# Performance work log

Measured on AMD Instinct MI355X. Metric: run time of the kernel, lower is better.

Reference implementation:

```python
import jax, jax.numpy as jnp
import numpy as np

N = 50000   # nodes
E = 800000  # edges
H = 64      # hidden channels
EPS = 1e-16  # PyG softmax denominator epsilon


def _ptconv(x, pos, src, dst, W_src, W_dst, W_val, W_pos, b_pos):
    """PyG PointTransformerConv: per-edge gather, positional MLP, vector
    attention (segment softmax over edges grouped by dst), scatter-sum.
    edge_index convention: src = j (neighbor), dst = i (center)."""
    a_src = x @ W_src          # [N,H] alpha_j projection
    a_dst = x @ W_dst          # [N,H] alpha_i projection
    v = x @ W_val              # [N,H] values
    # relative positional encoding: pos_nn(pos_i - pos_j), [E,H]
    delta = (pos[dst] - pos[src]) @ W_pos + b_pos
    alpha = a_dst[dst] - a_src[src] + delta           # [E,H]
    # numerically-stable vector softmax over variable-size neighborhoods
    m = jax.lax.stop_gradient(jax.ops.segment_max(alpha, dst, num_segments=N))
    e = jnp.exp(alpha - m[dst])
    s = jax.ops.segment_sum(e, dst, num_segments=N)
    attn = e / (s[dst] + EPS)                         # [E,H]
    return jax.ops.segment_sum(attn * (v[src] + delta), dst, num_segments=N)


def setup_inputs() -> dict:
    key = jax.random.key(0)
    ks = jax.random.split(key, 16)
    x = jax.random.normal(ks[0], (N, 3), dtype=jnp.float32)
    pos = jax.random.normal(ks[1], (N, 3), dtype=jnp.float32)
    edge_index = jax.random.randint(ks[2], (2, E), 0, N)
    batch = jnp.zeros((N,), dtype=jnp.int32)

    def lin(k, i, o):
        return (jax.random.normal(k, (i, o), dtype=jnp.float32)
                * np.float32(1.0 / np.sqrt(i)))

    return {
        "x": x, "pos": pos, "edge_index": edge_index, "batch": batch,
        # conv1 (in=3 -> H)
        "W1_src": lin(ks[3], 3, H), "W1_dst": lin(ks[4], 3, H),
        "W1_val": lin(ks[5], 3, H),
        "W1_pos": lin(ks[6], 3, H), "b1_pos": jnp.zeros((H,), jnp.float32),
        # conv2 (H -> H)
        "W2_src": lin(ks[7], H, H), "W2_dst": lin(ks[8], H, H),
        "W2_val": lin(ks[9], H, H),
        "W2_pos": lin(ks[10], 3, H), "b2_pos": jnp.zeros((H,), jnp.float32),
        # MLP head
        "W_fc1": lin(ks[11], H, H // 2), "b_fc1": jnp.zeros((H // 2,), jnp.float32),
        "W_fc2": lin(ks[12], H // 2, 1), "b_fc2": jnp.zeros((1,), jnp.float32),
    }


def reference(x, pos, edge_index, batch,
              W1_src, W1_dst, W1_val, W1_pos, b1_pos,
              W2_src, W2_dst, W2_val, W2_pos, b2_pos,
              W_fc1, b_fc1, W_fc2, b_fc2):
    src, dst = edge_index[0], edge_index[1]
    h = jax.nn.relu(_ptconv(x, pos, src, dst, W1_src, W1_dst, W1_val, W1_pos, b1_pos))
    h = jax.nn.relu(_ptconv(h, pos, src, dst, W2_src, W2_dst, W2_val, W2_pos, b2_pos))
    h = jax.nn.relu(h @ W_fc1 + b_fc1)
    return h @ W_fc2 + b_fc2  # [N, 1]
```

## Files before the change

### kernel.cpp

```cpp
#include <hip/hip_runtime.h>
#include <hip/hip_fp16.h>
#include <math.h>


#define HDIM 64

__global__ void zero_int_kernel(int* __restrict__ p, int n) {
    int i = blockIdx.x * blockDim.x + threadIdx.x;
    if (i < n) p[i] = 0;
}

__global__ void hist_rank_kernel(const int* __restrict__ dst, int* __restrict__ count,
                                 int* __restrict__ rank, int E) {
    int e = blockIdx.x * blockDim.x + threadIdx.x;
    if (e < E) rank[e] = atomicAdd(&count[dst[e]], 1);
}

__global__ void __launch_bounds__(256) scan_sum_kernel(
        const int* __restrict__ count, int* __restrict__ blocksum, int n) {
    __shared__ int wsum[4];
    int t = blockIdx.x * 256 + threadIdx.x;
    int base = t * 4;
    int s = 0;
    if (base + 3 < n) {
        int4 c = *(const int4*)&count[base];
        s = c.x + c.y + c.z + c.w;
    } else {
        for (int i = base; i < n; ++i) s += count[i];
    }
    #pragma unroll
    for (int off = 32; off >= 1; off >>= 1) s += __shfl_down(s, off);
    int lane = threadIdx.x & 63, wid = threadIdx.x >> 6;
    if (lane == 0) wsum[wid] = s;
    __syncthreads();
    if (threadIdx.x == 0)
        blocksum[blockIdx.x] = wsum[0] + wsum[1] + wsum[2] + wsum[3];
}

__global__ void scan_base_kernel(int* __restrict__ blocksum, int* __restrict__ offsets,
                                 int nblocks, int n) {
    int lane = threadIdx.x;
    int v = (lane < nblocks) ? blocksum[lane] : 0;
    int inc = v;
    #pragma unroll
    for (int off = 1; off < 64; off <<= 1) {
        int t = __shfl_up(inc, off);
        if (lane >= off) inc += t;
    }
    if (lane < nblocks) blocksum[lane] = inc - v;
    if (lane == 63) offsets[n] = inc;
}

__global__ void __launch_bounds__(256) scan_emit_kernel(
        const int* __restrict__ count, const int* __restrict__ blockbase,
        int* __restrict__ offsets, int n) {
    __shared__ int wpre[4];
    int t = blockIdx.x * 256 + threadIdx.x;
    int base = t * 4;
    int4 c = make_int4(0, 0, 0, 0);
    if (base + 3 < n) {
        c = *(const int4*)&count[base];
    } else {
        if (base + 0 < n) c.x = count[base + 0];
        if (base + 1 < n) c.y = count[base + 1];
        if (base + 2 < n) c.z = count[base + 2];
    }
    int tsum = c.x + c.y + c.z + c.w;
    int inc = tsum;
    int lane = threadIdx.x & 63, wid = threadIdx.x >> 6;
    #pragma unroll
    for (int off = 1; off < 64; off <<= 1) {
        int t2 = __shfl_up(inc, off);
        if (lane >= off) inc += t2;
    }
    if (lane == 63) wpre[wid] = inc;
    __syncthreads();
    int wbase = 0;
    for (int wq = 0; wq < wid; ++wq) wbase += wpre[wq];
    int excl = blockbase[blockIdx.x] + wbase + (inc - tsum);
    if (base + 0 < n) offsets[base + 0] = excl;
    if (base + 1 < n) offsets[base + 1] = excl + c.x;
    if (base + 2 < n) offsets[base + 2] = excl + c.x + c.y;
    if (base + 3 < n) offsets[base + 3] = excl + c.x + c.y + c.z;
}

__global__ void scatter_kernel(const int* __restrict__ src, const int* __restrict__ dst,
                               const int* __restrict__ rank, const int* __restrict__ offsets,
                               int* __restrict__ sorted_src, int E) {
    int e = blockIdx.x * blockDim.x + threadIdx.x;
    if (e < E) sorted_src[offsets[dst[e]] + rank[e]] = src[e];
}

__global__ void proj1_kernel(const float* __restrict__ x, const float* __restrict__ pos,
                             const float* __restrict__ Wsrc, const float* __restrict__ Wval,
                             const float* __restrict__ Wpos,
                             __half2* __restrict__ g, int N) {
    int t = blockIdx.x * blockDim.x + threadIdx.x;
    int node = t >> 6, c = t & 63;
    if (node >= N) return;
    float x0 = x[node * 3 + 0], x1 = x[node * 3 + 1], x2 = x[node * 3 + 2];
    float p0 = pos[node * 3 + 0], p1 = pos[node * 3 + 1], p2 = pos[node * 3 + 2];
    float as = fmaf(x0, Wsrc[c], fmaf(x1, Wsrc[64 + c], x2 * Wsrc[128 + c]));
    float vv = fmaf(x0, Wval[c], fmaf(x1, Wval[64 + c], x2 * Wval[128 + c]));
    float cc = fmaf(p0, Wpos[c], fmaf(p1, Wpos[64 + c], p2 * Wpos[128 + c]));
    g[node * 64 + c] = __float22half2_rn(make_float2(as + cc, vv - cc));
}

__global__ void __launch_bounds__(256) proj2_kernel(
        const float* __restrict__ h, const float* __restrict__ pos,
        const float* __restrict__ Wsrc, const float* __restrict__ Wval,
        const float* __restrict__ Wpos,
        __half2* __restrict__ g, int N) {
    __shared__ float Wsh[2 * 64 * 64];
    __shared__ float hrow[4][64];
    int tid = threadIdx.x;
    for (int idx = tid; idx < 4096; idx += 256) {
        Wsh[idx] = Wsrc[idx];
        Wsh[4096 + idx] = Wval[idx];
    }
    __syncthreads();
    int lane = tid & 63, wid = tid >> 6;
    float wp0 = Wpos[lane], wp1 = Wpos[64 + lane], wp2 = Wpos[128 + lane];
    int stride = gridDim.x * 4;
    for (int node = blockIdx.x * 4 + wid; node < N; node += stride) {
        hrow[wid][lane] = h[node * 64 + lane];
        float as = 0.f, vv = 0.f;
        #pragma unroll 8
        for (int k = 0; k < 64; ++k) {
            float hk = hrow[wid][k];
            as = fmaf(hk, Wsh[k * 64 + lane], as);
            vv = fmaf(hk, Wsh[4096 + k * 64 + lane], vv);
        }
        float p0 = pos[node * 3 + 0], p1 = pos[node * 3 + 1], p2 = pos[node * 3 + 2];
        float cc = fmaf(p0, wp0, fmaf(p1, wp1, p2 * wp2));
        g[node * 64 + lane] = __float22half2_rn(make_float2(as + cc, vv - cc));
    }
}

__device__ __forceinline__ void edge_acc(float d, __half2 gh, float& s, float& num) {
    float2 gv = __half22float2(gh);
    float ev = __expf(d - gv.x);
    s += ev;
    num = fmaf(ev, gv.y + d, num);
}

template <bool HEAD>
__global__ void __launch_bounds__(256) conv_edge_kernel(
        const float* __restrict__ pos,
        const int* __restrict__ offsets,
        const int* __restrict__ sorted_src,
        const __half2* __restrict__ g,
        const float* __restrict__ Wpos, const float* __restrict__ bpos,
        const float* __restrict__ Wfc1, const float* __restrict__ bfc1,
        const float* __restrict__ Wfc2, const float* __restrict__ bfc2,
        float* __restrict__ outbuf, int N) {
    int lane = threadIdx.x & 63;
    int wid = threadIdx.x >> 6;
    int node = __builtin_amdgcn_readfirstlane(blockIdx.x * 4 + wid);
    if (node >= N) return;

    float pdx = pos[node * 3 + 0], pdy = pos[node * 3 + 1], pdz = pos[node * 3 + 2];
    float d = fmaf(pdx, Wpos[lane],
              fmaf(pdy, Wpos[64 + lane],
              fmaf(pdz, Wpos[128 + lane], bpos[lane])));
    int beg = offsets[node], end = offsets[node + 1];

    float s0 = 0.f, n0 = 0.f, s1 = 0.f, n1 = 0.f;
    int e = beg;
    int aligned = min((beg + 3) & ~3, end);
    for (; e < aligned; ++e) {
        int i0 = __builtin_amdgcn_readfirstlane(sorted_src[e]);
        edge_acc(d, g[(size_t)i0 * 64 + lane], s0, n0);
    }
    for (; e + 4 <= end; e += 4) {
        int4 ii = *(const int4*)&sorted_src[e];
        int i0 = __builtin_amdgcn_readfirstlane(ii.x);
        int i1 = __builtin_amdgcn_readfirstlane(ii.y);
        int i2 = __builtin_amdgcn_readfirstlane(ii.z);
        int i3 = __builtin_amdgcn_readfirstlane(ii.w);
        __half2 g0 = g[(size_t)i0 * 64 + lane];
        __half2 g1 = g[(size_t)i1 * 64 + lane];
        __half2 g2 = g[(size_t)i2 * 64 + lane];
        __half2 g3 = g[(size_t)i3 * 64 + lane];
        edge_acc(d, g0, s0, n0);
        edge_acc(d, g1, s1, n1);
        edge_acc(d, g2, s0, n0);
        edge_acc(d, g3, s1, n1);
    }
    for (; e < end; ++e) {
        int i0 = __builtin_amdgcn_readfirstlane(sorted_src[e]);
        edge_acc(d, g[(size_t)i0 * 64 + lane], s0, n0);
    }
    float s = s0 + s1;
    float num = n0 + n1;
    float hval = fmaxf(num / (s + 1e-16f), 0.f);

    if (!HEAD) {
        outbuf[node * 64 + lane] = hval;
    } else {
        __shared__ float hsh[4][64];
        hsh[wid][lane] = hval;
        float t = 0.f;
        if (lane < 32) {
            #pragma unroll
            for (int k = 0; k < 64; ++k) t = fmaf(hsh[wid][k], Wfc1[k * 32 + lane], t);
            t += bfc1[lane];
            t = fmaxf(t, 0.f);
            t *= Wfc2[lane];
        }
        #pragma unroll
        for (int off = 32; off >= 1; off >>= 1) t += __shfl_down(t, off);
        if (lane == 0) outbuf[node] = t + bfc2[0];
    }
}

extern "C" void kernel_launch(void* const* d_in, const int* in_sizes, int n_in,
                              void* d_out, int out_size, void* d_ws, size_t ws_size,
                              hipStream_t stream) {
    const float* x   = (const float*)d_in[0];
    const float* pos = (const float*)d_in[1];
    const int* eidx  = (const int*)d_in[2];
    const float* W1_src = (const float*)d_in[4];
    const float* W1_val = (const float*)d_in[6];
    const float* W1_pos = (const float*)d_in[7];
    const float* b1_pos = (const float*)d_in[8];
    const float* W2_src = (const float*)d_in[9];
    const float* W2_val = (const float*)d_in[11];
    const float* W2_pos = (const float*)d_in[12];
    const float* b2_pos = (const float*)d_in[13];
    const float* W_fc1  = (const float*)d_in[14];
    const float* b_fc1  = (const float*)d_in[15];
    const float* W_fc2  = (const float*)d_in[16];
    const float* b_fc2  = (const float*)d_in[17];

    const int N = in_sizes[0] / 3;
    const int E = in_sizes[2] / 2;
    const int* src = eidx;
    const int* dst = eidx + E;

    char* w = (char*)d_ws;
    auto carve = [&](size_t bytes) -> void* {
        void* p = (void*)w;
        w += (bytes + 255) & ~size_t(255);
        return p;
    };
    const int nsb = (N + 1023) / 1024;
    int*     count      = (int*)carve((size_t)N * 4);
    int*     offsets    = (int*)carve((size_t)(N + 1) * 4);
    int*     blocksum   = (int*)carve((size_t)nsb * 4);
    int*     rank       = (int*)carve((size_t)E * 4);
    int*     sorted_src = (int*)carve((size_t)E * 4);
    __half2* g          = (__half2*)carve((size_t)N * HDIM * 4);
    float*   h          = (float*)carve((size_t)N * HDIM * 4);

    zero_int_kernel<<<(N + 255) / 256, 256, 0, stream>>>(count, N);
    hist_rank_kernel<<<(E + 255) / 256, 256, 0, stream>>>(dst, count, rank, E);
    scan_sum_kernel<<<nsb, 256, 0, stream>>>(count, blocksum, N);
    scan_base_kernel<<<1, 64, 0, stream>>>(blocksum, offsets, nsb, N);
    scan_emit_kernel<<<nsb, 256, 0, stream>>>(count, blocksum, offsets, N);
    scatter_kernel<<<(E + 255) / 256, 256, 0, stream>>>(src, dst, rank, offsets,
                                                        sorted_src, E);

    proj1_kernel<<<(N * 64 + 255) / 256, 256, 0, stream>>>(x, pos, W1_src, W1_val,
                                                           W1_pos, g, N);
    conv_edge_kernel<false><<<(N + 3) / 4, 256, 0, stream>>>(
        pos, offsets, sorted_src, g, W1_pos, b1_pos,
        W_fc1, b_fc1, W_fc2, b_fc2, h, N);

    proj2_kernel<<<1024, 256, 0, stream>>>(h, pos, W2_src, W2_val, W2_pos, g, N);
    conv_edge_kernel<true><<<(N + 3) / 4, 256, 0, stream>>>(
        pos, offsets, sorted_src, g, W2_pos, b2_pos,
        W_fc1, b_fc1, W_fc2, b_fc2, (float*)d_out, N);
}
```

Baseline: 277.5 us.

## Fuse projection stages into edge kernels and merge scan/histogram launches

Fuses the layer-2 projection into the layer-1 edge aggregation kernel, so h never goes to global memory; the matmul reads from shuffles and half2 weights held in shared memory. Merges the histogram with the layer-1 projection and folds the scan-base step into scan_emit, which cuts the launch count. Also pre-scales logits by log2e so the inner loop can use exp2f, unrolls the edge loop by 8, and loads the head weights into shared memory. In exchange, W2 weights are now stored in fp16, the fused kernel uses more shared memory per block, and the scan fold assumes nsb is at most 64.

```diff
diff --git a/kernel.cpp b/kernel.cpp
--- a/kernel.cpp
+++ b/kernel.cpp
@@ -3,24 +3,34 @@
 #include <math.h>
 
 
-#define HDIM 64
-
-__global__ void zero_int_kernel(int* __restrict__ p, int n) {
-    int i = blockIdx.x * blockDim.x + threadIdx.x;
-    if (i < n) p[i] = 0;
-}
-
-__global__ void hist_rank_kernel(const int* __restrict__ dst, int* __restrict__ count,
-                                 int* __restrict__ rank, int E) {
-    int e = blockIdx.x * blockDim.x + threadIdx.x;
-    if (e < E) rank[e] = atomicAdd(&count[dst[e]], 1);
+#define LOG2E 1.44269504088896340736f
+
+__global__ void __launch_bounds__(256) hist_proj1_kernel(
+        const int* __restrict__ dst, int* __restrict__ count, int* __restrict__ rank,
+        const float* __restrict__ x, const float* __restrict__ pos,
+        const float* __restrict__ W1_src, const float* __restrict__ W1_val,
+        const float* __restrict__ W1_pos,
+        __half2* __restrict__ g1, int N, int E) {
+    int gtid = blockIdx.x * 256 + threadIdx.x;
+    int gsz = gridDim.x * 256;
+    for (int e = gtid; e < E; e += gsz)
+        rank[e] = atomicAdd(&count[dst[e]], 1);
+    for (int t = gtid; t < N * 64; t += gsz) {
+        int node = t >> 6, c = t & 63;
+        float x0 = x[node * 3 + 0], x1 = x[node * 3 + 1], x2 = x[node * 3 + 2];
+        float p0 = pos[node * 3 + 0], p1 = pos[node * 3 + 1], p2 = pos[node * 3 + 2];
+        float as = fmaf(x0, W1_src[c], fmaf(x1, W1_src[64 + c], x2 * W1_src[128 + c]));
+        float vv = fmaf(x0, W1_val[c], fmaf(x1, W1_val[64 + c], x2 * W1_val[128 + c]));
+        float cc = fmaf(p0, W1_pos[c], fmaf(p1, W1_pos[64 + c], p2 * W1_pos[128 + c]));
+        g1[t] = __floats2half2_rn((as + cc) * LOG2E, vv - cc);
+    }
 }
 
 __global__ void __launch_bounds__(256) scan_sum_kernel(
         const int* __restrict__ count, int* __restrict__ blocksum, int n) {
     __shared__ int wsum[4];
-    int t = blockIdx.x * 256 + threadIdx.x;
-    int base = t * 4;
+    int tid = threadIdx.x;
+    int base = (blockIdx.x * 256 + tid) * 4;
     int s = 0;
     if (base + 3 < n) {
         int4 c = *(const int4*)&count[base];
@@ -30,33 +40,30 @@
     }
     #pragma unroll
     for (int off = 32; off >= 1; off >>= 1) s += __shfl_down(s, off);
-    int lane = threadIdx.x & 63, wid = threadIdx.x >> 6;
+    int lane = tid & 63, wid = tid >> 6;
     if (lane == 0) wsum[wid] = s;
     __syncthreads();
-    if (threadIdx.x == 0)
-        blocksum[blockIdx.x] = wsum[0] + wsum[1] + wsum[2] + wsum[3];
-}
-
-__global__ void scan_base_kernel(int* __restrict__ blocksum, int* __restrict__ offsets,
-                                 int nblocks, int n) {
-    int lane = threadIdx.x;
-    int v = (lane < nblocks) ? blocksum[lane] : 0;
-    int inc = v;
-    #pragma unroll
-    for (int off = 1; off < 64; off <<= 1) {
-        int t = __shfl_up(inc, off);
-        if (lane >= off) inc += t;
-    }
-    if (lane < nblocks) blocksum[lane] = inc - v;
-    if (lane == 63) offsets[n] = inc;
+    if (tid == 0) blocksum[blockIdx.x] = wsum[0] + wsum[1] + wsum[2] + wsum[3];
 }
 
 __global__ void __launch_bounds__(256) scan_emit_kernel(
-        const int* __restrict__ count, const int* __restrict__ blockbase,
-        int* __restrict__ offsets, int n) {
+        const int* __restrict__ count, const int* __restrict__ blocksum,
+        int* __restrict__ offsets, int n, int nsb) {
     __shared__ int wpre[4];
-    int t = blockIdx.x * 256 + threadIdx.x;
-    int base = t * 4;
+    __shared__ int sbase[2];
+    int tid = threadIdx.x, lane = tid & 63, wid = tid >> 6;
+    if (tid < 64) {
+        int v = (lane < nsb) ? blocksum[lane] : 0;
+        int inc = v;
+        #pragma unroll
+        for (int off = 1; off < 64; off <<= 1) {
+            int t2 = __shfl_up(inc, off);
+            if (lane >= off) inc += t2;
+        }
+        if (lane == (int)blockIdx.x) sbase[0] = inc - v;
+        if (lane == nsb - 1) sbase[1] = inc;
+    }
+    int base = (blockIdx.x * 256 + tid) * 4;
     int4 c = make_int4(0, 0, 0, 0);
     if (base + 3 < n) {
         c = *(const int4*)&count[base];
@@ -67,7 +74,6 @@
     }
     int tsum = c.x + c.y + c.z + c.w;
     int inc = tsum;
-    int lane = threadIdx.x & 63, wid = threadIdx.x >> 6;
     #pragma unroll
     for (int off = 1; off < 64; off <<= 1) {
         int t2 = __shfl_up(inc, off);
@@ -76,142 +82,165 @@
     if (lane == 63) wpre[wid] = inc;
     __syncthreads();
     int wbase = 0;
-    for (int wq = 0; wq < wid; ++wq) wbase += wpre[wq];
-    int excl = blockbase[blockIdx.x] + wbase + (inc - tsum);
+    for (int q = 0; q < wid; ++q) wbase += wpre[q];
+    int excl = sbase[0] + wbase + (inc - tsum);
     if (base + 0 < n) offsets[base + 0] = excl;
     if (base + 1 < n) offsets[base + 1] = excl + c.x;
     if (base + 2 < n) offsets[base + 2] = excl + c.x + c.y;
     if (base + 3 < n) offsets[base + 3] = excl + c.x + c.y + c.z;
-}
-
-__global__ void scatter_kernel(const int* __restrict__ src, const int* __restrict__ dst,
-                               const int* __restrict__ rank, const int* __restrict__ offsets,
-                               int* __restrict__ sorted_src, int E) {
-    int e = blockIdx.x * blockDim.x + threadIdx.x;
+    if (blockIdx.x == 0 && tid == 0) offsets[n] = sbase[1];
+}
+
+__global__ void __launch_bounds__(256) scatter_kernel(
+        const int* __restrict__ src, const int* __restrict__ dst,
+        const int* __restrict__ rank, const int* __restrict__ offsets,
+        int* __restrict__ sorted_src, int E) {
+    int e = blockIdx.x * 256 + threadIdx.x;
     if (e < E) sorted_src[offsets[dst[e]] + rank[e]] = src[e];
 }
 
-__global__ void proj1_kernel(const float* __restrict__ x, const float* __restrict__ pos,
-                             const float* __restrict__ Wsrc, const float* __restrict__ Wval,
-                             const float* __restrict__ Wpos,
-                             __half2* __restrict__ g, int N) {
-    int t = blockIdx.x * blockDim.x + threadIdx.x;
-    int node = t >> 6, c = t & 63;
-    if (node >= N) return;
-    float x0 = x[node * 3 + 0], x1 = x[node * 3 + 1], x2 = x[node * 3 + 2];
-    float p0 = pos[node * 3 + 0], p1 = pos[node * 3 + 1], p2 = pos[node * 3 + 2];
-    float as = fmaf(x0, Wsrc[c], fmaf(x1, Wsrc[64 + c], x2 * Wsrc[128 + c]));
-    float vv = fmaf(x0, Wval[c], fmaf(x1, Wval[64 + c], x2 * Wval[128 + c]));
-    float cc = fmaf(p0, Wpos[c], fmaf(p1, Wpos[64 + c], p2 * Wpos[128 + c]));
-    g[node * 64 + c] = __float22half2_rn(make_float2(as + cc, vv - cc));
-}
-
-__global__ void __launch_bounds__(256) proj2_kernel(
-        const float* __restrict__ h, const float* __restrict__ pos,
-        const float* __restrict__ Wsrc, const float* __restrict__ Wval,
-        const float* __restrict__ Wpos,
-        __half2* __restrict__ g, int N) {
-    __shared__ float Wsh[2 * 64 * 64];
-    __shared__ float hrow[4][64];
-    int tid = threadIdx.x;
-    for (int idx = tid; idx < 4096; idx += 256) {
-        Wsh[idx] = Wsrc[idx];
-        Wsh[4096 + idx] = Wval[idx];
-    }
-    __syncthreads();
-    int lane = tid & 63, wid = tid >> 6;
-    float wp0 = Wpos[lane], wp1 = Wpos[64 + lane], wp2 = Wpos[128 + lane];
-    int stride = gridDim.x * 4;
-    for (int node = blockIdx.x * 4 + wid; node < N; node += stride) {
-        hrow[wid][lane] = h[node * 64 + lane];
-        float as = 0.f, vv = 0.f;
-        #pragma unroll 8
-        for (int k = 0; k < 64; ++k) {
-            float hk = hrow[wid][k];
-            as = fmaf(hk, Wsh[k * 64 + lane], as);
-            vv = fmaf(hk, Wsh[4096 + k * 64 + lane], vv);
-        }
-        float p0 = pos[node * 3 + 0], p1 = pos[node * 3 + 1], p2 = pos[node * 3 + 2];
-        float cc = fmaf(p0, wp0, fmaf(p1, wp1, p2 * wp2));
-        g[node * 64 + lane] = __float22half2_rn(make_float2(as + cc, vv - cc));
-    }
-}
-
-__device__ __forceinline__ void edge_acc(float d, __half2 gh, float& s, float& num) {
-    float2 gv = __half22float2(gh);
-    float ev = __expf(d - gv.x);
+__device__ __forceinline__ void eacc(float d2, float dv, __half2 gh,
+                                     float& s, float& num) {
+    float ax = __low2float(gh);
+    float vv = __high2float(gh);
+    float ev = exp2f(d2 - ax);
     s += ev;
-    num = fmaf(ev, gv.y + d, num);
-}
-
-template <bool HEAD>
-__global__ void __launch_bounds__(256) conv_edge_kernel(
-        const float* __restrict__ pos,
-        const int* __restrict__ offsets,
-        const int* __restrict__ sorted_src,
-        const __half2* __restrict__ g,
-        const float* __restrict__ Wpos, const float* __restrict__ bpos,
-        const float* __restrict__ Wfc1, const float* __restrict__ bfc1,
-        const float* __restrict__ Wfc2, const float* __restrict__ bfc2,
-        float* __restrict__ outbuf, int N) {
-    int lane = threadIdx.x & 63;
-    int wid = threadIdx.x >> 6;
-    int node = __builtin_amdgcn_readfirstlane(blockIdx.x * 4 + wid);
-    if (node >= N) return;
-
-    float pdx = pos[node * 3 + 0], pdy = pos[node * 3 + 1], pdz = pos[node * 3 + 2];
-    float d = fmaf(pdx, Wpos[lane],
-              fmaf(pdy, Wpos[64 + lane],
-              fmaf(pdz, Wpos[128 + lane], bpos[lane])));
+    num = fmaf(ev, vv + dv, num);
+}
+
+__device__ __forceinline__ float edge_node(
+        int node, int laneoff,
+        const int* __restrict__ offsets, const int* __restrict__ ss,
+        const char* __restrict__ gbase, float d2, float dv) {
     int beg = offsets[node], end = offsets[node + 1];
-
     float s0 = 0.f, n0 = 0.f, s1 = 0.f, n1 = 0.f;
     int e = beg;
     int aligned = min((beg + 3) & ~3, end);
     for (; e < aligned; ++e) {
-        int i0 = __builtin_amdgcn_readfirstlane(sorted_src[e]);
-        edge_acc(d, g[(size_t)i0 * 64 + lane], s0, n0);
+        int i0 = __builtin_amdgcn_readfirstlane(ss[e]);
+        __half2 g0 = *(const __half2*)(gbase + (((size_t)(unsigned)i0) << 8) + laneoff);
+        eacc(d2, dv, g0, s0, n0);
+    }
+    for (; e + 8 <= end; e += 8) {
+        int4 ia = *(const int4*)(ss + e);
+        int4 ib = *(const int4*)(ss + e + 4);
+        int i0 = __builtin_amdgcn_readfirstlane(ia.x);
+        int i1 = __builtin_amdgcn_readfirstlane(ia.y);
+        int i2 = __builtin_amdgcn_readfirstlane(ia.z);
+        int i3 = __builtin_amdgcn_readfirstlane(ia.w);
+        int i4 = __builtin_amdgcn_readfirstlane(ib.x);
+        int i5 = __builtin_amdgcn_readfirstlane(ib.y);
+        int i6 = __builtin_amdgcn_readfirstlane(ib.z);
+        int i7 = __builtin_amdgcn_readfirstlane(ib.w);
+        __half2 g0 = *(const __half2*)(gbase + (((size_t)(unsigned)i0) << 8) + laneoff);
+        __half2 g1 = *(const __half2*)(gbase + (((size_t)(unsigned)i1) << 8) + laneoff);
+        __half2 g2 = *(const __half2*)(gbase + (((size_t)(unsigned)i2) << 8) + laneoff);
+        __half2 g3 = *(const __half2*)(gbase + (((size_t)(unsigned)i3) << 8) + laneoff);
+        __half2 g4 = *(const __half2*)(gbase + (((size_t)(unsigned)i4) << 8) + laneoff);
+        __half2 g5 = *(const __half2*)(gbase + (((size_t)(unsigned)i5) << 8) + laneoff);
+        __half2 g6 = *(const __half2*)(gbase + (((size_t)(unsigned)i6) << 8) + laneoff);
+        __half2 g7 = *(const __half2*)(gbase + (((size_t)(unsigned)i7) << 8) + laneoff);
+        eacc(d2, dv, g0, s0, n0);
+        eacc(d2, dv, g1, s1, n1);
+        eacc(d2, dv, g2, s0, n0);
+        eacc(d2, dv, g3, s1, n1);
+        eacc(d2, dv, g4, s0, n0);
+        eacc(d2, dv, g5, s1, n1);
+        eacc(d2, dv, g6, s0, n0);
+        eacc(d2, dv, g7, s1, n1);
     }
     for (; e + 4 <= end; e += 4) {
-        int4 ii = *(const int4*)&sorted_src[e];
-        int i0 = __builtin_amdgcn_readfirstlane(ii.x);
-        int i1 = __builtin_amdgcn_readfirstlane(ii.y);
-        int i2 = __builtin_amdgcn_readfirstlane(ii.z);
-        int i3 = __builtin_amdgcn_readfirstlane(ii.w);
-        __half2 g0 = g[(size_t)i0 * 64 + lane];
-        __half2 g1 = g[(size_t)i1 * 64 + lane];
-        __half2 g2 = g[(size_t)i2 * 64 + lane];
-        __half2 g3 = g[(size_t)i3 * 64 + lane];
-        edge_acc(d, g0, s0, n0);
-        edge_acc(d, g1, s1, n1);
-        edge_acc(d, g2, s0, n0);
-        edge_acc(d, g3, s1, n1);
+        int4 ia = *(const int4*)(ss + e);
+        int i0 = __builtin_amdgcn_readfirstlane(ia.x);
+        int i1 = __builtin_amdgcn_readfirstlane(ia.y);
+        int i2 = __builtin_amdgcn_readfirstlane(ia.z);
+        int i3 = __builtin_amdgcn_readfirstlane(ia.w);
+        __half2 g0 = *(const __half2*)(gbase + (((size_t)(unsigned)i0) << 8) + laneoff);
+        __half2 g1 = *(const __half2*)(gbase + (((size_t)(unsigned)i1) << 8) + laneoff);
+        __half2 g2 = *(const __half2*)(gbase + (((size_t)(unsigned)i2) << 8) + laneoff);
+        __half2 g3 = *(const __half2*)(gbase + (((size_t)(unsigned)i3) << 8) + laneoff);
+        eacc(d2, dv, g0, s0, n0);
+        eacc(d2, dv, g1, s1, n1);
+        eacc(d2, dv, g2, s0, n0);
+        eacc(d2, dv, g3, s1, n1);
     }
     for (; e < end; ++e) {
-        int i0 = __builtin_amdgcn_readfirstlane(sorted_src[e]);
-        edge_acc(d, g[(size_t)i0 * 64 + lane], s0, n0);
-    }
-    float s = s0 + s1;
-    float num = n0 + n1;
-    float hval = fmaxf(num / (s + 1e-16f), 0.f);
-
-    if (!HEAD) {
-        outbuf[node * 64 + lane] = hval;
-    } else {
-        __shared__ float hsh[4][64];
-        hsh[wid][lane] = hval;
-        float t = 0.f;
-        if (lane < 32) {
-            #pragma unroll
-            for (int k = 0; k < 64; ++k) t = fmaf(hsh[wid][k], Wfc1[k * 32 + lane], t);
-            t += bfc1[lane];
-            t = fmaxf(t, 0.f);
-            t *= Wfc2[lane];
-        }
-        #pragma unroll
-        for (int off = 32; off >= 1; off >>= 1) t += __shfl_down(t, off);
-        if (lane == 0) outbuf[node] = t + bfc2[0];
-    }
+        int i0 = __builtin_amdgcn_readfirstlane(ss[e]);
+        __half2 g0 = *(const __half2*)(gbase + (((size_t)(unsigned)i0) << 8) + laneoff);
+        eacc(d2, dv, g0, s0, n0);
+    }
+    return fmaxf((n0 + n1) / (s0 + s1 + 1e-16f), 0.f);
+}
+
+__global__ void __launch_bounds__(256, 8) e1p2_kernel(
+        const float* __restrict__ pos,
+        const int* __restrict__ offsets, const int* __restrict__ sorted_src,
+        const __half2* __restrict__ g1,
+        const float* __restrict__ W1_pos, const float* __restrict__ b1_pos,
+        const float* __restrict__ W2_src, const float* __restrict__ W2_val,
+        const float* __restrict__ W2_pos,
+        __half2* __restrict__ g2, int N) {
+    __shared__ __half2 Wsh[4096];
+    int tid = threadIdx.x, lane = tid & 63, wid = tid >> 6;
+    for (int idx = tid; idx < 4096; idx += 256)
+        Wsh[idx] = __floats2half2_rn(W2_src[idx], W2_val[idx]);
+    __syncthreads();
+
+    int node = blockIdx.x * 4 + wid;
+    if (node >= N) return;
+
+    float p0 = pos[node * 3 + 0], p1 = pos[node * 3 + 1], p2 = pos[node * 3 + 2];
+    float dpos = fmaf(p0, W1_pos[lane],
+                 fmaf(p1, W1_pos[64 + lane], p2 * W1_pos[128 + lane]));
+    float hval = edge_node(node, lane * 4, offsets, sorted_src,
+                           (const char*)g1, dpos * LOG2E, dpos + b1_pos[lane]);
+    float as = 0.f, vv = 0.f;
+    #pragma unroll 16
+    for (int k = 0; k < 64; ++k) {
+        float hk = __shfl(hval, k);
+        float2 wk = __half22float2(Wsh[k * 64 + lane]);
+        as = fmaf(hk, wk.x, as);
+        vv = fmaf(hk, wk.y, vv);
+    }
+    float cc = fmaf(p0, W2_pos[lane],
+               fmaf(p1, W2_pos[64 + lane], p2 * W2_pos[128 + lane]));
+    g2[node * 64 + lane] = __floats2half2_rn((as + cc) * LOG2E, vv - cc);
+}
+
+__global__ void __launch_bounds__(256, 8) e2head_kernel(
+        const float* __restrict__ pos,
+        const int* __restrict__ offsets, const int* __restrict__ sorted_src,
+        const __half2* __restrict__ g2,
+        const float* __restrict__ W2_pos, const float* __restrict__ b2_pos,
+        const float* __restrict__ Wfc1, const float* __restrict__ bfc1,
+        const float* __restrict__ Wfc2, const float* __restrict__ bfc2,
+        float* __restrict__ out, int N) {
+    __shared__ float Wfc1sh[64 * 32];
+    __shared__ float hsh[4][64];
+    int tid = threadIdx.x, lane = tid & 63, wid = tid >> 6;
+    for (int idx = tid; idx < 2048; idx += 256) Wfc1sh[idx] = Wfc1[idx];
+    __syncthreads();
+
+    int node = blockIdx.x * 4 + wid;
+    if (node >= N) return;
+
+    float p0 = pos[node * 3 + 0], p1 = pos[node * 3 + 1], p2 = pos[node * 3 + 2];
+    float dpos = fmaf(p0, W2_pos[lane],
+                 fmaf(p1, W2_pos[64 + lane], p2 * W2_pos[128 + lane]));
+    float hval = edge_node(node, lane * 4, offsets, sorted_src,
+                           (const char*)g2, dpos * LOG2E, dpos + b2_pos[lane]);
+    hsh[wid][lane] = hval;
+    int c = lane & 31, kh = (lane >> 5) * 32;
+    float t2 = 0.f;
+    #pragma unroll 8
+    for (int k = 0; k < 32; ++k)
+        t2 = fmaf(hsh[wid][kh + k], Wfc1sh[(kh + k) * 32 + c], t2);
+    t2 += __shfl_down(t2, 32);
+    t2 = fmaxf(t2 + bfc1[c], 0.f) * Wfc2[c];
+    t2 = (lane < 32) ? t2 : 0.f;
+    #pragma unroll
+    for (int off = 16; off >= 1; off >>= 1) t2 += __shfl_down(t2, off);
+    if (lane == 0) out[node] = t2 + bfc2[0];
 }
 
 extern "C" void kernel_launch(void* const* d_in, const int* in_sizes, int n_in,
@@ -237,6 +266,7 @@
     const int E = in_sizes[2] / 2;
     const int* src = eidx;
     const int* dst = eidx + E;
+    const int nsb = (N + 1023) / 1024;
 
     char* w = (char*)d_ws;
     auto carve = [&](size_t bytes) -> void* {
@@ -244,31 +274,24 @@
         w += (bytes + 255) & ~size_t(255);
         return p;
     };
-    const int nsb = (N + 1023) / 1024;
     int*     count      = (int*)carve((size_t)N * 4);
     int*     offsets    = (int*)carve((size_t)(N + 1) * 4);
-    int*     blocksum   = (int*)carve((size_t)nsb * 4);
+    int*     blocksum   = (int*)carve((size_t)64 * 4);
     int*     rank       = (int*)carve((size_t)E * 4);
     int*     sorted_src = (int*)carve((size_t)E * 4);
-    __half2* g          = (__half2*)carve((size_t)N * HDIM * 4);
-    float*   h          = (float*)carve((size_t)N * HDIM * 4);
-
-    zero_int_kernel<<<(N + 255) / 256, 256, 0, stream>>>(count, N);
-    hist_rank_kernel<<<(E + 255) / 256, 256, 0, stream>>>(dst, count, rank, E);
+    __half2* g1         = (__half2*)carve((size_t)N * 64 * 4);
+    __half2* g2         = (__half2*)carve((size_t)N * 64 * 4);
+
+    hipMemsetAsync(count, 0, (size_t)N * 4, stream);
+    hist_proj1_kernel<<<(N * 64 + 255) / 256, 256, 0, stream>>>(
+        dst, count, rank, x, pos, W1_src, W1_val, W1_pos, g1, N, E);
     scan_sum_kernel<<<nsb, 256, 0, stream>>>(count, blocksum, N);
-    scan_base_kernel<<<1, 64, 0, stream>>>(blocksum, offsets, nsb, N);
-    scan_emit_kernel<<<nsb, 256, 0, stream>>>(count, blocksum, offsets, N);
+    scan_emit_kernel<<<nsb, 256, 0, stream>>>(count, blocksum, offsets, N, nsb);
     scatter_kernel<<<(E + 255) / 256, 256, 0, stream>>>(src, dst, rank, offsets,
                                                         sorted_src, E);
-
-    proj1_kernel<<<(N * 64 + 255) / 256, 256, 0, stream>>>(x, pos, W1_src, W1_val,
-                                                           W1_pos, g, N);
-    conv_edge_kernel<false><<<(N + 3) / 4, 256, 0, stream>>>(
-        pos, offsets, sorted_src, g, W1_pos, b1_pos,
-        W_fc1, b_fc1, W_fc2, b_fc2, h, N);
-
-    proj2_kernel<<<1024, 256, 0, stream>>>(h, pos, W2_src, W2_val, W2_pos, g, N);
-    conv_edge_kernel<true><<<(N + 3) / 4, 256, 0, stream>>>(
-        pos, offsets, sorted_src, g, W2_pos, b2_pos,
+    e1p2_kernel<<<(N + 3) / 4, 256, 0, stream>>>(
+        pos, offsets, sorted_src, g1, W1_pos, b1_pos, W2_src, W2_val, W2_pos, g2, N);
+    e2head_kernel<<<(N + 3) / 4, 256, 0, stream>>>(
+        pos, offsets, sorted_src, g2, W2_pos, b2_pos,
         W_fc1, b_fc1, W_fc2, b_fc2, (float*)d_out, N);
 }
```

Result: slower. 287.6 us (+3.7%).
